# Performance work log

Hardware: AMD Instinct MI355X
Metric: run time of the kernel (lower is better)

Reference implementation:

```python
import jax, jax.numpy as jnp
import numpy as np

N_NODES = 100000
N_EDGES = 1600000
D_IN = 128
D_H = 128
N_CLASSES = 64


def setup_inputs() -> dict:
    key = jax.random.key(0)
    ks = jax.random.split(key, 8)
    feat = jax.random.normal(ks[0], (N_NODES, D_IN), dtype=jnp.float32)
    src = jax.random.randint(ks[1], (N_EDGES,), 0, N_NODES)
    dst = jax.random.randint(ks[2], (N_EDGES,), 0, N_NODES)
    # Xavier-ish scaled weights (nn.Linear layout: [out, in])
    W1 = jax.random.normal(ks[3], (D_H, D_IN), dtype=jnp.float32) * (1.0 / np.sqrt(D_IN))
    b1 = jnp.zeros((D_H,), dtype=jnp.float32)
    W2 = jax.random.normal(ks[4], (D_H, D_H), dtype=jnp.float32) * (1.0 / np.sqrt(D_H))
    b2 = jnp.zeros((D_H,), dtype=jnp.float32)
    Wl = jax.random.normal(ks[5], (N_CLASSES, 2 * D_H), dtype=jnp.float32) * (1.0 / np.sqrt(2 * D_H))
    bl = jnp.zeros((N_CLASSES,), dtype=jnp.float32)
    return {"feat": feat, "src": src, "dst": dst, "W1": W1, "b1": b1,
            "W2": W2, "b2": b2, "Wl": Wl, "bl": bl}


def _mean_agg(h, src, dst, inv_deg, n):
    # copy_u('h','m') + mean('m','neigh'): gather src features, segment-sum on dst, divide by in-degree
    s = jax.ops.segment_sum(h[src], dst, num_segments=n)  # [N, D]
    return s * inv_deg


def reference(feat, src, dst, W1, b1, W2, b2, Wl, bl):
    n = feat.shape[0]
    deg = jax.ops.segment_sum(jnp.ones_like(dst, dtype=feat.dtype), dst, num_segments=n)
    inv_deg = (1.0 / jnp.maximum(deg, 1.0))[:, None]  # zero-degree nodes -> 0 (sum is 0 anyway)
    h1 = jax.nn.relu(_mean_agg(feat, src, dst, inv_deg, n) @ W1.T + b1)
    h2 = jax.nn.relu(_mean_agg(h1, src, dst, inv_deg, n) @ W2.T + b2)
    logits = jnp.concatenate([h1, h2], axis=-1) @ Wl.T + bl
    return jax.nn.log_softmax(logits, axis=-1)
```

## Files before the change

kernel.cpp:

```cpp
#include <hip/hip_runtime.h>
#include <hip/hip_fp8.h>
#include <stdint.h>

#define D 128
#define NCLS 64
#define BSH 7
#define NBMAX 1024
#define CCHUNK 4096
#define HISTB 256
#define GEMMB 2048

typedef __bf16 bf16x8 __attribute__((ext_vector_type(8)));
typedef float f32x4 __attribute__((ext_vector_type(4)));
typedef float f32x2 __attribute__((ext_vector_type(2)));

union B8 { uint4 u; bf16x8 v; };

__device__ __forceinline__ B8 pack8(const float4& a, const float4& b) {
  union { __bf16 h[8]; uint4 u; } p;
  p.h[0] = (__bf16)a.x; p.h[1] = (__bf16)a.y; p.h[2] = (__bf16)a.z; p.h[3] = (__bf16)a.w;
  p.h[4] = (__bf16)b.x; p.h[5] = (__bf16)b.y; p.h[6] = (__bf16)b.z; p.h[7] = (__bf16)b.w;
  B8 r; r.u = p.u; return r;
}


__global__ __launch_bounds__(256) void k_pre(const int* __restrict__ dst,
                                             const float* __restrict__ feat,
                                             const float* __restrict__ W1,
                                             int* __restrict__ bcnt,
                                             unsigned char* __restrict__ Z,
                                             int N, int E, int NB) {
  __shared__ int h[NBMAX];
  if (blockIdx.x < HISTB) {
    for (int i = threadIdx.x; i < NB; i += 256) h[i] = 0;
    __syncthreads();
    for (int e = blockIdx.x * 256 + threadIdx.x; e < E; e += HISTB * 256)
      atomicAdd(&h[dst[e] >> BSH], 1);
    __syncthreads();
    for (int i = threadIdx.x; i < NB; i += 256) {
      int c = h[i];
      if (c) atomicAdd(&bcnt[i], c);
    }
    return;
  }
  const int bid = blockIdx.x - HISTB;
  const int wave = threadIdx.x >> 6;
  const int lane = threadIdx.x & 63;
  const int l15 = lane & 15;
  const int quad = lane >> 4;

  B8 bfrag[2][4];
#pragma unroll
  for (int t = 0; t < 2; ++t) {
    const int n = wave * 32 + t * 16 + l15;
    const float* wp = W1 + (size_t)n * D + quad * 8;
#pragma unroll
    for (int ks = 0; ks < 4; ++ks)
      bfrag[t][ks] = pack8(*reinterpret_cast<const float4*>(wp + ks * 32),
                           *reinterpret_cast<const float4*>(wp + ks * 32 + 4));
  }

  const int mtiles = (N + 15) >> 4;
  for (int mt = bid; mt < mtiles; mt += GEMMB) {
    const int arow = min(mt * 16 + l15, N - 1);
    const float* ap = feat + (size_t)arow * D + quad * 8;
    B8 a[4];
#pragma unroll
    for (int ks = 0; ks < 4; ++ks)
      a[ks] = pack8(*reinterpret_cast<const float4*>(ap + ks * 32),
                    *reinterpret_cast<const float4*>(ap + ks * 32 + 4));
#pragma unroll
    for (int t = 0; t < 2; ++t) {
      f32x4 acc = {0.f, 0.f, 0.f, 0.f};
#pragma unroll
      for (int ks = 0; ks < 4; ++ks)
        acc = __builtin_amdgcn_mfma_f32_16x16x32_bf16(a[ks].v, bfrag[t][ks].v, acc, 0, 0, 0);
      const int col = wave * 32 + t * 16 + l15;
#pragma unroll
      for (int r = 0; r < 4; ++r) {
        const int orow = mt * 16 + quad * 4 + r;
        if (orow < N) {
          __hip_fp8_e4m3 q((float)acc[r]);
          Z[(size_t)orow * D + col] = q.__x;
        }
      }
    }
  }
}


__global__ __launch_bounds__(1024) void k_bscan(const int* __restrict__ bcnt,
                                                int* __restrict__ bbase,
                                                int* __restrict__ bcur, int NB, int E) {
  __shared__ int sm[NBMAX];
  const int tid = threadIdx.x;
  int v = (tid < NB) ? bcnt[tid] : 0;
  sm[tid] = v;
  __syncthreads();
  for (int off = 1; off < NBMAX; off <<= 1) {
    int t = (tid >= off) ? sm[tid - off] : 0;
    __syncthreads();
    sm[tid] += t;
    __syncthreads();
  }
  if (tid < NB) {
    bbase[tid] = sm[tid] - v;
    bcur[tid] = sm[tid] - v;
  }
  if (tid == 0) bbase[NB] = E;
}

__global__ __launch_bounds__(256) void k_bscatter(const int* __restrict__ src,
                                                  const int* __restrict__ dst,
                                                  int* __restrict__ bcur,
                                                  int* __restrict__ ebuck, int E, int NB) {
  __shared__ int h[NBMAX];
  __shared__ int base[NBMAX];
  const int beg = blockIdx.x * CCHUNK;
  const int end = min(beg + CCHUNK, E);
  for (int i = threadIdx.x; i < NB; i += 256) h[i] = 0;
  __syncthreads();
  for (int e = beg + threadIdx.x; e < end; e += 256)
    atomicAdd(&h[dst[e] >> BSH], 1);
  __syncthreads();
  for (int i = threadIdx.x; i < NB; i += 256) {
    int c = h[i];
    base[i] = c ? atomicAdd(&bcur[i], c) : 0;
    h[i] = 0;
  }
  __syncthreads();
  for (int e = beg + threadIdx.x; e < end; e += 256) {
    const int d = dst[e];
    const int b = d >> BSH;
    const int r = atomicAdd(&h[b], 1);
    ebuck[base[b] + r] = (src[e] << BSH) | (d & 127);
  }
}

__global__ __launch_bounds__(256) void k_bbuild(const int* __restrict__ ebuck,
                                                const int* __restrict__ bbase,
                                                int* __restrict__ row_ptr,
                                                int* __restrict__ esrc,
                                                float* __restrict__ inv, int N, int E) {
  __shared__ int cnt[128], s[128], cur[128];
  const int b = blockIdx.x;
  const int n0 = b << BSH;
  const int nn = min(128, N - n0);
  const int beg = bbase[b], end = bbase[b + 1];
  const int tid = threadIdx.x;
  if (tid < 128) cnt[tid] = 0;
  __syncthreads();
  for (int e = beg + tid; e < end; e += 256)
    atomicAdd(&cnt[ebuck[e] & 127], 1);
  __syncthreads();
  if (tid < 128) s[tid] = cnt[tid];
  __syncthreads();
  for (int off = 1; off < 128; off <<= 1) {
    int t = (tid < 128 && tid >= off) ? s[tid - off] : 0;
    __syncthreads();
    if (tid < 128) s[tid] += t;
    __syncthreads();
  }
  if (tid < 128) {
    const int ex = s[tid] - cnt[tid];
    cur[tid] = ex;
    if (tid < nn) {
      row_ptr[n0 + tid] = beg + ex;
      inv[n0 + tid] = 1.0f / fmaxf((float)cnt[tid], 1.0f);
    }
  }
  if (b == 0 && tid == 0) row_ptr[N] = E;
  __syncthreads();
  for (int e = beg + tid; e < end; e += 256) {
    const int p = ebuck[e];
    const int r = atomicAdd(&cur[p & 127], 1);
    esrc[beg + r] = p >> BSH;
  }
}


__global__ __launch_bounds__(256) void k_gemmz2(const ushort* __restrict__ A,
                                                const float* __restrict__ W,
                                                unsigned char* __restrict__ Z, int N) {
  const int wave = threadIdx.x >> 6;
  const int lane = threadIdx.x & 63;
  const int l15 = lane & 15;
  const int quad = lane >> 4;

  B8 bfrag[2][4];
#pragma unroll
  for (int t = 0; t < 2; ++t) {
    const int n = wave * 32 + t * 16 + l15;
    const float* wp = W + (size_t)n * D + quad * 8;
#pragma unroll
    for (int ks = 0; ks < 4; ++ks)
      bfrag[t][ks] = pack8(*reinterpret_cast<const float4*>(wp + ks * 32),
                           *reinterpret_cast<const float4*>(wp + ks * 32 + 4));
  }

  const int mtiles = (N + 15) >> 4;
  for (int mt = blockIdx.x; mt < mtiles; mt += gridDim.x) {
    const int arow = min(mt * 16 + l15, N - 1);
    const ushort* ap = A + (size_t)arow * D + quad * 8;
    B8 a[4];
#pragma unroll
    for (int ks = 0; ks < 4; ++ks)
      a[ks].u = *reinterpret_cast<const uint4*>(ap + ks * 32);
#pragma unroll
    for (int t = 0; t < 2; ++t) {
      f32x4 acc = {0.f, 0.f, 0.f, 0.f};
#pragma unroll
      for (int ks = 0; ks < 4; ++ks)
        acc = __builtin_amdgcn_mfma_f32_16x16x32_bf16(a[ks].v, bfrag[t][ks].v, acc, 0, 0, 0);
      const int col = wave * 32 + t * 16 + l15;
#pragma unroll
      for (int r = 0; r < 4; ++r) {
        const int orow = mt * 16 + quad * 4 + r;
        if (orow < N) {
          __hip_fp8_e4m3 q((float)acc[r]);
          Z[(size_t)orow * D + col] = q.__x;
        }
      }
    }
  }
}


__device__ __forceinline__ void accq8(f32x2 acc[4], const uint2& u) {
  union { uint2 v; unsigned char b[8]; } t;
  t.v = u;
#pragma unroll
  for (int i = 0; i < 4; ++i) {
    __hip_fp8_e4m3 f0, f1;
    f0.__x = t.b[2 * i];
    f1.__x = t.b[2 * i + 1];
    f32x2 d;
    d.x = (float)f0;
    d.y = (float)f1;
    acc[i] += d;
  }
}

__device__ __forceinline__ void gather_acc8(const unsigned char* __restrict__ hp,
                                            const int* __restrict__ esrc,
                                            int beg, int end, f32x2 acc[4]) {
  int e = beg;
  for (; e + 3 < end; e += 4) {
    const int4 ss = *reinterpret_cast<const int4*>(esrc + e);
    const uint2 u0 = *reinterpret_cast<const uint2*>(hp + (size_t)ss.x * D);
    const uint2 u1 = *reinterpret_cast<const uint2*>(hp + (size_t)ss.y * D);
    const uint2 u2 = *reinterpret_cast<const uint2*>(hp + (size_t)ss.z * D);
    const uint2 u3 = *reinterpret_cast<const uint2*>(hp + (size_t)ss.w * D);
    accq8(acc, u0);
    accq8(acc, u1);
    accq8(acc, u2);
    accq8(acc, u3);
  }
  for (; e < end; ++e) {
    const int s0 = esrc[e];
    const uint2 u0 = *reinterpret_cast<const uint2*>(hp + (size_t)s0 * D);
    accq8(acc, u0);
  }
}


__global__ __launch_bounds__(256) void k_gather_relu(const unsigned char* __restrict__ z,
                                                     const int* __restrict__ row_ptr,
                                                     const int* __restrict__ esrc,
                                                     const float* __restrict__ inv,
                                                     const float* __restrict__ bias,
                                                     ushort* __restrict__ out, int N) {
  const int g = threadIdx.x >> 4;
  const int w = threadIdx.x & 15;
  const unsigned char* hp = z + w * 8;
  float bb[8];
  {
    const float4 x = *reinterpret_cast<const float4*>(bias + w * 8);
    const float4 y = *reinterpret_cast<const float4*>(bias + w * 8 + 4);
    bb[0] = x.x; bb[1] = x.y; bb[2] = x.z; bb[3] = x.w;
    bb[4] = y.x; bb[5] = y.y; bb[6] = y.z; bb[7] = y.w;
  }
  const int ntiles = (N + 15) >> 4;
  for (int tile = blockIdx.x; tile < ntiles; tile += gridDim.x) {
    const int node = tile * 16 + g;
    if (node >= N) continue;
    f32x2 acc[4] = {{0.f, 0.f}, {0.f, 0.f}, {0.f, 0.f}, {0.f, 0.f}};
    gather_acc8(hp, esrc, row_ptr[node], row_ptr[node + 1], acc);
    const float iv = inv[node];
    union { __bf16 b[8]; uint4 u; } p;
#pragma unroll
    for (int i = 0; i < 4; ++i) {
      p.b[i * 2 + 0] = (__bf16)fmaxf(acc[i].x * iv + bb[i * 2 + 0], 0.f);
      p.b[i * 2 + 1] = (__bf16)fmaxf(acc[i].y * iv + bb[i * 2 + 1], 0.f);
    }
    *reinterpret_cast<uint4*>(out + (size_t)node * D + w * 8) = p.u;
  }
}


__global__ __launch_bounds__(256, 2) void k_logits(const ushort* __restrict__ h1,
                                                   const ushort* __restrict__ h2,
                                                   const float* __restrict__ Wl,
                                                   const float* __restrict__ bl,
                                                   float* __restrict__ out, int N) {
  const int lane = threadIdx.x & 63;
  const int l15 = lane & 15;
  const int quad = lane >> 4;
  const int wid = blockIdx.x * 4 + (threadIdx.x >> 6);
  const int nw = gridDim.x * 4;

  B8 wfrag[4][8];
  float blv[4];
#pragma unroll
  for (int t = 0; t < 4; ++t) {
    const int n = t * 16 + l15;
    blv[t] = bl[n];
    const float* wp = Wl + (size_t)n * (2 * D) + quad * 8;
#pragma unroll
    for (int ks = 0; ks < 8; ++ks)
      wfrag[t][ks] = pack8(*reinterpret_cast<const float4*>(wp + ks * 32),
                           *reinterpret_cast<const float4*>(wp + ks * 32 + 4));
  }

  const int mtiles = (N + 15) >> 4;
  for (int mt = wid; mt < mtiles; mt += nw) {
    const int arow = min(mt * 16 + l15, N - 1);
    const ushort* p1 = h1 + (size_t)arow * D + quad * 8;
    const ushort* p2 = h2 + (size_t)arow * D + quad * 8;
    B8 a1[4], a2[4];
#pragma unroll
    for (int ks = 0; ks < 4; ++ks) {
      a1[ks].u = *reinterpret_cast<const uint4*>(p1 + ks * 32);
      a2[ks].u = *reinterpret_cast<const uint4*>(p2 + ks * 32);
    }
    f32x4 acc[4];
#pragma unroll
    for (int t = 0; t < 4; ++t) acc[t] = f32x4{0.f, 0.f, 0.f, 0.f};
#pragma unroll
    for (int ks = 0; ks < 4; ++ks)
#pragma unroll
      for (int t = 0; t < 4; ++t)
        acc[t] = __builtin_amdgcn_mfma_f32_16x16x32_bf16(a1[ks].v, wfrag[t][ks].v, acc[t], 0, 0, 0);
#pragma unroll
    for (int ks = 0; ks < 4; ++ks)
#pragma unroll
      for (int t = 0; t < 4; ++t)
        acc[t] = __builtin_amdgcn_mfma_f32_16x16x32_bf16(a2[ks].v, wfrag[t][4 + ks].v, acc[t], 0, 0, 0);
#pragma unroll
    for (int t = 0; t < 4; ++t)
#pragma unroll
      for (int r = 0; r < 4; ++r)
        acc[t][r] += blv[t];
#pragma unroll
    for (int r = 0; r < 4; ++r) {
      float m = fmaxf(fmaxf(acc[0][r], acc[1][r]), fmaxf(acc[2][r], acc[3][r]));
#pragma unroll
      for (int off = 8; off > 0; off >>= 1) m = fmaxf(m, __shfl_xor(m, off));
      const float e0 = __expf(acc[0][r] - m);
      const float e1 = __expf(acc[1][r] - m);
      const float e2 = __expf(acc[2][r] - m);
      const float e3 = __expf(acc[3][r] - m);
      float s = (e0 + e1) + (e2 + e3);
#pragma unroll
      for (int off = 8; off > 0; off >>= 1) s += __shfl_xor(s, off);
      const float ls = m + __logf(s);
      const int orow = mt * 16 + quad * 4 + r;
      if (orow < N) {
        float* op = out + (size_t)orow * NCLS + l15;
#pragma unroll
        for (int t = 0; t < 4; ++t) op[t * 16] = acc[t][r] - ls;
      }
    }
  }
}


extern "C" void kernel_launch(void* const* d_in, const int* in_sizes, int n_in,
                              void* d_out, int out_size, void* d_ws, size_t ws_size,
                              hipStream_t stream) {
  const float* feat = (const float*)d_in[0];
  const int* src = (const int*)d_in[1];
  const int* dst = (const int*)d_in[2];
  const float* W1 = (const float*)d_in[3];
  const float* b1 = (const float*)d_in[4];
  const float* W2 = (const float*)d_in[5];
  const float* b2 = (const float*)d_in[6];
  const float* Wl = (const float*)d_in[7];
  const float* bl = (const float*)d_in[8];
  float* out = (float*)d_out;

  const int N = in_sizes[0] / D;
  const int E = in_sizes[1];
  const int NB = (N + 127) >> BSH;

  float* ws = (float*)d_ws;
  float* inv = ws;
  ushort* h1b = (ushort*)(inv + N);
  ushort* h2b = h1b + (size_t)N * D;
  unsigned char* z8 = (unsigned char*)(h2b + (size_t)N * D);
  int* row_ptr = (int*)(z8 + (size_t)N * D);
  int* esrc = row_ptr + N + 1;
  int* ebuck = esrc + E;
  int* bcnt = ebuck + E;
  int* bbase = bcnt + NBMAX;
  int* bcur = bbase + NBMAX + 1;

  hipMemsetAsync(bcnt, 0, NBMAX * sizeof(int), stream);

  k_pre<<<HISTB + GEMMB, 256, 0, stream>>>(dst, feat, W1, bcnt, z8, N, E, NB);

  k_bscan<<<1, 1024, 0, stream>>>(bcnt, bbase, bcur, NB, E);
  k_bscatter<<<(E + CCHUNK - 1) / CCHUNK, 256, 0, stream>>>(src, dst, bcur, ebuck, E, NB);
  k_bbuild<<<NB, 256, 0, stream>>>(ebuck, bbase, row_ptr, esrc, inv, N, E);

  k_gather_relu<<<2048, 256, 0, stream>>>(z8, row_ptr, esrc, inv, b1, h1b, N);

  k_gemmz2<<<2048, 256, 0, stream>>>(h1b, W2, z8, N);
  k_gather_relu<<<2048, 256, 0, stream>>>(z8, row_ptr, esrc, inv, b2, h2b, N);

  k_logits<<<512, 256, 0, stream>>>(h1b, h2b, Wl, bl, out, N);
}
```

Before: 361.7 us.

## Use packed fp8 conversion builtins and register-cache edges in CSR build kernels

Swaps the scalar hip_fp8 conversions for packed hardware builtins, cvt_pk_fp8_f32 when storing GEMM output and cvt_pk_f32_fp8 when decoding in the gather loop. This is meant to cut the ALU work of the per-byte conversion. The scatter and bucket-build kernels now load each edge into registers once and reuse it across the histogram and placement passes, and the scatter chunk size is halved. The gather loop also prefetches the next group of source indices. Risks include rounding and saturation differences from the hardware fp8 conversion, and extra register pressure.

```diff
diff --git a/kernel.cpp b/kernel.cpp
--- a/kernel.cpp
+++ b/kernel.cpp
@@ -1,12 +1,11 @@
 #include <hip/hip_runtime.h>
-#include <hip/hip_fp8.h>
 #include <stdint.h>
 
 #define D 128
 #define NCLS 64
 #define BSH 7
 #define NBMAX 1024
-#define CCHUNK 4096
+#define CCHUNK 2048
 #define HISTB 256
 #define GEMMB 2048
 
@@ -21,6 +20,20 @@
   p.h[0] = (__bf16)a.x; p.h[1] = (__bf16)a.y; p.h[2] = (__bf16)a.z; p.h[3] = (__bf16)a.w;
   p.h[4] = (__bf16)b.x; p.h[5] = (__bf16)b.y; p.h[6] = (__bf16)b.z; p.h[7] = (__bf16)b.w;
   B8 r; r.u = p.u; return r;
+}
+
+__device__ __forceinline__ void store_fp8_rows(unsigned char* __restrict__ Z,
+                                               const f32x4& acc, int row0, int col, int N) {
+  const int p01 = __builtin_amdgcn_cvt_pk_fp8_f32(acc[0], acc[1], 0, false);
+  const int p23 = __builtin_amdgcn_cvt_pk_fp8_f32(acc[2], acc[3], 0, false);
+  const unsigned char b0 = (unsigned char)(p01 & 0xff);
+  const unsigned char b1 = (unsigned char)((p01 >> 8) & 0xff);
+  const unsigned char b2 = (unsigned char)(p23 & 0xff);
+  const unsigned char b3 = (unsigned char)((p23 >> 8) & 0xff);
+  if (row0 + 0 < N) Z[(size_t)(row0 + 0) * D + col] = b0;
+  if (row0 + 1 < N) Z[(size_t)(row0 + 1) * D + col] = b1;
+  if (row0 + 2 < N) Z[(size_t)(row0 + 2) * D + col] = b2;
+  if (row0 + 3 < N) Z[(size_t)(row0 + 3) * D + col] = b3;
 }
 
 
@@ -75,15 +88,7 @@
 #pragma unroll
       for (int ks = 0; ks < 4; ++ks)
         acc = __builtin_amdgcn_mfma_f32_16x16x32_bf16(a[ks].v, bfrag[t][ks].v, acc, 0, 0, 0);
-      const int col = wave * 32 + t * 16 + l15;
-#pragma unroll
-      for (int r = 0; r < 4; ++r) {
-        const int orow = mt * 16 + quad * 4 + r;
-        if (orow < N) {
-          __hip_fp8_e4m3 q((float)acc[r]);
-          Z[(size_t)orow * D + col] = q.__x;
-        }
-      }
+      store_fp8_rows(Z, acc, mt * 16 + quad * 4, wave * 32 + t * 16 + l15, N);
     }
   }
 }
@@ -116,24 +121,35 @@
                                                   int* __restrict__ ebuck, int E, int NB) {
   __shared__ int h[NBMAX];
   __shared__ int base[NBMAX];
+  const int tid = threadIdx.x;
   const int beg = blockIdx.x * CCHUNK;
   const int end = min(beg + CCHUNK, E);
-  for (int i = threadIdx.x; i < NB; i += 256) h[i] = 0;
-  __syncthreads();
-  for (int e = beg + threadIdx.x; e < end; e += 256)
-    atomicAdd(&h[dst[e] >> BSH], 1);
-  __syncthreads();
-  for (int i = threadIdx.x; i < NB; i += 256) {
-    int c = h[i];
+  int d[8];
+#pragma unroll
+  for (int i = 0; i < 8; ++i) {
+    const int e = beg + i * 256 + tid;
+    d[i] = (e < end) ? dst[e] : -1;
+  }
+  for (int i = tid; i < NB; i += 256) h[i] = 0;
+  __syncthreads();
+#pragma unroll
+  for (int i = 0; i < 8; ++i)
+    if (d[i] >= 0) atomicAdd(&h[d[i] >> BSH], 1);
+  __syncthreads();
+  for (int i = tid; i < NB; i += 256) {
+    const int c = h[i];
     base[i] = c ? atomicAdd(&bcur[i], c) : 0;
     h[i] = 0;
   }
   __syncthreads();
-  for (int e = beg + threadIdx.x; e < end; e += 256) {
-    const int d = dst[e];
-    const int b = d >> BSH;
-    const int r = atomicAdd(&h[b], 1);
-    ebuck[base[b] + r] = (src[e] << BSH) | (d & 127);
+#pragma unroll
+  for (int i = 0; i < 8; ++i) {
+    if (d[i] >= 0) {
+      const int e = beg + i * 256 + tid;
+      const int b = d[i] >> BSH;
+      const int r = atomicAdd(&h[b], 1);
+      ebuck[base[b] + r] = (src[e] << BSH) | (d[i] & 127);
+    }
   }
 }
 
@@ -148,9 +164,18 @@
   const int nn = min(128, N - n0);
   const int beg = bbase[b], end = bbase[b + 1];
   const int tid = threadIdx.x;
+  int v[12];
+#pragma unroll
+  for (int i = 0; i < 12; ++i) {
+    const int e = beg + i * 256 + tid;
+    v[i] = (e < end) ? ebuck[e] : -1;
+  }
   if (tid < 128) cnt[tid] = 0;
   __syncthreads();
-  for (int e = beg + tid; e < end; e += 256)
+#pragma unroll
+  for (int i = 0; i < 12; ++i)
+    if (v[i] >= 0) atomicAdd(&cnt[v[i] & 127], 1);
+  for (int e = beg + 3072 + tid; e < end; e += 256)
     atomicAdd(&cnt[ebuck[e] & 127], 1);
   __syncthreads();
   if (tid < 128) s[tid] = cnt[tid];
@@ -171,7 +196,13 @@
   }
   if (b == 0 && tid == 0) row_ptr[N] = E;
   __syncthreads();
-  for (int e = beg + tid; e < end; e += 256) {
+#pragma unroll
+  for (int i = 0; i < 12; ++i)
+    if (v[i] >= 0) {
+      const int r = atomicAdd(&cur[v[i] & 127], 1);
+      esrc[beg + r] = v[i] >> BSH;
+    }
+  for (int e = beg + 3072 + tid; e < end; e += 256) {
     const int p = ebuck[e];
     const int r = atomicAdd(&cur[p & 127], 1);
     esrc[beg + r] = p >> BSH;
@@ -212,54 +243,42 @@
 #pragma unroll
       for (int ks = 0; ks < 4; ++ks)
         acc = __builtin_amdgcn_mfma_f32_16x16x32_bf16(a[ks].v, bfrag[t][ks].v, acc, 0, 0, 0);
-      const int col = wave * 32 + t * 16 + l15;
-#pragma unroll
-      for (int r = 0; r < 4; ++r) {
-        const int orow = mt * 16 + quad * 4 + r;
-        if (orow < N) {
-          __hip_fp8_e4m3 q((float)acc[r]);
-          Z[(size_t)orow * D + col] = q.__x;
-        }
-      }
-    }
-  }
-}
-
-
-__device__ __forceinline__ void accq8(f32x2 acc[4], const uint2& u) {
-  union { uint2 v; unsigned char b[8]; } t;
-  t.v = u;
-#pragma unroll
-  for (int i = 0; i < 4; ++i) {
-    __hip_fp8_e4m3 f0, f1;
-    f0.__x = t.b[2 * i];
-    f1.__x = t.b[2 * i + 1];
-    f32x2 d;
-    d.x = (float)f0;
-    d.y = (float)f1;
-    acc[i] += d;
-  }
+      store_fp8_rows(Z, acc, mt * 16 + quad * 4, wave * 32 + t * 16 + l15, N);
+    }
+  }
+}
+
+
+__device__ __forceinline__ void accq8pk(f32x2 acc[4], const uint2& u) {
+  acc[0] += __builtin_amdgcn_cvt_pk_f32_fp8((int)u.x, false);
+  acc[1] += __builtin_amdgcn_cvt_pk_f32_fp8((int)u.x, true);
+  acc[2] += __builtin_amdgcn_cvt_pk_f32_fp8((int)u.y, false);
+  acc[3] += __builtin_amdgcn_cvt_pk_f32_fp8((int)u.y, true);
 }
 
 __device__ __forceinline__ void gather_acc8(const unsigned char* __restrict__ hp,
                                             const int* __restrict__ esrc,
                                             int beg, int end, f32x2 acc[4]) {
+  const int n4 = (end - beg) >> 2;
   int e = beg;
-  for (; e + 3 < end; e += 4) {
-    const int4 ss = *reinterpret_cast<const int4*>(esrc + e);
-    const uint2 u0 = *reinterpret_cast<const uint2*>(hp + (size_t)ss.x * D);
-    const uint2 u1 = *reinterpret_cast<const uint2*>(hp + (size_t)ss.y * D);
-    const uint2 u2 = *reinterpret_cast<const uint2*>(hp + (size_t)ss.z * D);
-    const uint2 u3 = *reinterpret_cast<const uint2*>(hp + (size_t)ss.w * D);
-    accq8(acc, u0);
-    accq8(acc, u1);
-    accq8(acc, u2);
-    accq8(acc, u3);
+  if (n4 > 0) {
+    int4 ss = *reinterpret_cast<const int4*>(esrc + e);
+    for (int it = 0; it < n4; ++it) {
+      const uint2 u0 = *reinterpret_cast<const uint2*>(hp + (size_t)ss.x * D);
+      const uint2 u1 = *reinterpret_cast<const uint2*>(hp + (size_t)ss.y * D);
+      const uint2 u2 = *reinterpret_cast<const uint2*>(hp + (size_t)ss.z * D);
+      const uint2 u3 = *reinterpret_cast<const uint2*>(hp + (size_t)ss.w * D);
+      e += 4;
+      if (it + 1 < n4) ss = *reinterpret_cast<const int4*>(esrc + e);
+      accq8pk(acc, u0);
+      accq8pk(acc, u1);
+      accq8pk(acc, u2);
+      accq8pk(acc, u3);
+    }
   }
   for (; e < end; ++e) {
-    const int s0 = esrc[e];
-    const uint2 u0 = *reinterpret_cast<const uint2*>(hp + (size_t)s0 * D);
-    accq8(acc, u0);
+    const uint2 u0 = *reinterpret_cast<const uint2*>(hp + (size_t)esrc[e] * D);
+    accq8pk(acc, u0);
   }
 }
 
```

New measurement: 346.0 us. 1.05x faster.
